# Kernel tuning notes

Measured on AMD Instinct MI355X. Metric: run time of the kernel, lower is better.

The kernel has to match this reference:

```python
import jax, jax.numpy as jnp
import numpy as np

N_NODES = 100000
N_EDGES = 1600000
NFEAT = 128
NHID = 128


def setup_inputs() -> dict:
    key = jax.random.key(0)
    k1, k2, k3, k4 = jax.random.split(key, 4)
    x = jax.random.normal(k1, (N_NODES, NFEAT), dtype=jnp.float32)
    edge_index = jax.random.randint(k2, (2, N_EDGES), 0, N_NODES, dtype=jnp.int64)
    # GCNConv params (glorot-style scale)
    W1 = jax.random.normal(k3, (NFEAT, NHID), dtype=jnp.float32) * (1.0 / np.sqrt(NFEAT))
    b1 = jnp.zeros((NHID,), dtype=jnp.float32)
    return {"x": x, "edge_index": edge_index, "W1": W1, "b1": b1}


def gcn_conv(x, edge_index, W, b):
    # PyG GCNConv: out = D^{-1/2} (A + I) D^{-1/2} (x W) + b
    n = x.shape[0]
    loop = jnp.arange(n, dtype=edge_index.dtype)
    src = jnp.concatenate([edge_index[0], loop])  # message sources
    dst = jnp.concatenate([edge_index[1], loop])  # aggregation targets
    deg = jax.ops.segment_sum(jnp.ones_like(dst, dtype=x.dtype), dst, num_segments=n)
    dinv = jnp.where(deg > 0, jax.lax.rsqrt(deg), 0.0)
    norm = dinv[src] * dinv[dst]  # [E+N]
    h = x @ W  # [N, nhid]
    msg = h[src] * norm[:, None]  # gather + scale, [E+N, nhid]
    out = jax.ops.segment_sum(msg, dst, num_segments=n) + b
    return out


def reference(x, edge_index, W1, b1):
    # forward = gc1(x, edge_index) followed by dropout (identity in eval mode)
    return gcn_conv(x, edge_index, W1, b1)
```

## Files before the change

### kernel.cpp

```cpp
#include <hip/hip_runtime.h>
#include <math.h>


#define N_NODES 100000
#define N_EDGES 1600000
#define NF 128

#define BSHIFT 7
#define BNODES 128
#define NBUCK 782
#define ECAP 2432
#define CHUNK 4096
#define NCHUNK 391
#define GEMM_BLOCKS 1563

typedef short bf16x8 __attribute__((ext_vector_type(8)));
typedef float f32x4  __attribute__((ext_vector_type(4)));
typedef unsigned short u16;

__device__ inline u16 f2bf(float f) {
    unsigned int u = __float_as_uint(f);
    return (u16)((u + 0x7fffu + ((u >> 16) & 1u)) >> 16);
}

__device__ inline f32x4 unpk4u(unsigned int u) {
    f32x4 r;
    r[0] = (float)(u & 0xffu);
    r[1] = (float)((u >> 8) & 0xffu);
    r[2] = (float)((u >> 16) & 0xffu);
    r[3] = (float)((u >> 24) & 0xffu);
    return r;
}

__global__ __launch_bounds__(256) void prep_kernel(const float* __restrict__ W,
                                                   u16* __restrict__ Wimg,
                                                   int* __restrict__ bcur) {
    const int t = threadIdx.x;
    if (blockIdx.x == 0)
        for (int b = t; b < NBUCK; b += 256) bcur[b] = 0;
    for (int idx = blockIdx.x * 256 + t; idx < NF * NF; idx += 16 * 256) {
        int n = idx >> 7, k = idx & 127;
        Wimg[idx] = f2bf(W[k * NF + n]);
    }
}

__global__ __launch_bounds__(256, 4) void fused1_kernel(const float* __restrict__ x,
                                                        const u16* __restrict__ Wimg,
                                                        signed char* __restrict__ h8,
                                                        float* __restrict__ rscale,
                                                        const int* __restrict__ ei,
                                                        int* __restrict__ bcur,
                                                        unsigned int* __restrict__ ebuf) {
    __shared__ __align__(16) char smem[22656];
    const int t = threadIdx.x;

    if (blockIdx.x >= GEMM_BLOCKS) {
        unsigned int* ed = (unsigned int*)smem;
        int* cnt = (int*)(smem + 16384);
        int* cur = (int*)(smem + 16384 + 3136);
        const int c = blockIdx.x - GEMM_BLOCKS;
        for (int b = t; b < NBUCK; b += 256) cnt[b] = 0;
        const int e0 = c * CHUNK;
        #pragma unroll 4
        for (int it = 0; it < CHUNK / 256; ++it) {
            int k = it * 256 + t, e = e0 + k;
            ed[k] = (e < N_EDGES) ? (unsigned int)ei[N_EDGES + e] : 0xFFFFFFFFu;
        }
        __syncthreads();
        #pragma unroll 4
        for (int it = 0; it < CHUNK / 256; ++it) {
            unsigned int d = ed[it * 256 + t];
            if (d != 0xFFFFFFFFu) atomicAdd(&cnt[d >> BSHIFT], 1);
        }
        __syncthreads();
        for (int b = t; b < NBUCK; b += 256) {
            int v = cnt[b];
            cur[b] = b * ECAP + (v ? atomicAdd(&bcur[b], v) : 0);
        }
        __syncthreads();
        #pragma unroll 4
        for (int it = 0; it < CHUNK / 256; ++it) {
            int k = it * 256 + t;
            unsigned int d = ed[k];
            if (d != 0xFFFFFFFFu) {
                int pos = atomicAdd(&cur[d >> BSHIFT], 1);
                ebuf[pos] = ((d & (BNODES - 1u)) << 17) | (unsigned int)ei[e0 + k];
            }
        }
        return;
    }

    const int lane = t & 63;
    const int w = t >> 6;
    const int quad = lane >> 4;
    const int m = lane & 15;
    const int rowbase = blockIdx.x * 64;
    const int r0 = w * 16;
    const int arow = rowbase + r0 + m;
    const bool rv = arow < N_NODES;
    const float4* x4 = (const float4*)x;

    f32x4 acc[8];
    #pragma unroll
    for (int nt = 0; nt < 8; ++nt) acc[nt] = (f32x4){0.f, 0.f, 0.f, 0.f};

    #pragma unroll
    for (int kt = 0; kt < 4; ++kt) {
        float4 xa = make_float4(0.f, 0.f, 0.f, 0.f), xb = xa;
        if (rv) {
            xa = x4[arow * 32 + kt * 8 + quad * 2];
            xb = x4[arow * 32 + kt * 8 + quad * 2 + 1];
        }
        bf16x8 a;
        a[0] = (short)f2bf(xa.x); a[1] = (short)f2bf(xa.y);
        a[2] = (short)f2bf(xa.z); a[3] = (short)f2bf(xa.w);
        a[4] = (short)f2bf(xb.x); a[5] = (short)f2bf(xb.y);
        a[6] = (short)f2bf(xb.z); a[7] = (short)f2bf(xb.w);
        #pragma unroll
        for (int nt = 0; nt < 8; ++nt) {
            bf16x8 bb = *(const bf16x8*)&Wimg[(nt * 16 + m) * NF + kt * 32 + quad * 8];
            acc[nt] = __builtin_amdgcn_mfma_f32_16x16x32_bf16(a, bb, acc[nt], 0, 0, 0);
        }
    }

    float rmax[4];
    #pragma unroll
    for (int r = 0; r < 4; ++r) {
        float mx = 0.f;
        #pragma unroll
        for (int nt = 0; nt < 8; ++nt) mx = fmaxf(mx, fabsf(acc[nt][r]));
        #pragma unroll
        for (int off = 1; off < 16; off <<= 1) mx = fmaxf(mx, __shfl_xor(mx, off));
        rmax[r] = fmaxf(mx, 1e-20f);
    }

    char* xs8 = smem;
    #pragma unroll
    for (int r = 0; r < 4; ++r) {
        const float inv = 127.f / rmax[r];
        const int row = r0 + quad * 4 + r;
        #pragma unroll
        for (int nt = 0; nt < 8; ++nt) {
            int q = __float2int_rn(acc[nt][r] * inv) + 128;
            xs8[row * 144 + nt * 16 + m] = (char)q;
        }
        if (m == 0) {
            int grow = rowbase + row;
            if (grow < N_NODES) rscale[grow] = rmax[r] * (1.f / 127.f);
        }
    }
    __syncthreads();

    for (int it = 0; it < 2; ++it) {
        int linear = it * 256 + t;
        int row = linear >> 3, seg = linear & 7;
        int grow = rowbase + row;
        if (grow < N_NODES) {
            uint4 v = *(const uint4*)&xs8[row * 144 + seg * 16];
            ((uint4*)h8)[grow * 8 + seg] = v;
        }
    }
}

__global__ __launch_bounds__(256) void fill3_kernel(unsigned int* __restrict__ ebuf,
                                                    const int* __restrict__ bcur,
                                                    const float* __restrict__ rscale,
                                                    float* __restrict__ combo,
                                                    int4* __restrict__ nodetab) {
    __shared__ unsigned int lde[ECAP];
    __shared__ int lcnt[BNODES];
    __shared__ int lsc[BNODES];
    __shared__ int lcur[BNODES];
    const int t = threadIdx.x, bkt = blockIdx.x;
    const int cnt = min(bcur[bkt], ECAP);
    const int gbase = bkt * ECAP;
    if (t < BNODES) lcnt[t] = 0;
    __syncthreads();
    for (int e = t; e < cnt; e += 256) {
        unsigned int p = ebuf[gbase + e];
        lde[e] = p;
        atomicAdd(&lcnt[p >> 17], 1);
    }
    __syncthreads();
    if (t < BNODES) lsc[t] = lcnt[t];
    __syncthreads();
    #pragma unroll
    for (int off = 1; off < BNODES; off <<= 1) {
        int v = (t < BNODES) ? lsc[t] : 0;
        int add = (t >= off && t < BNODES) ? lsc[t - off] : 0;
        __syncthreads();
        if (t < BNODES) lsc[t] = v + add;
        __syncthreads();
    }
    if (t < BNODES) {
        int c = lcnt[t];
        int startp = gbase + lsc[t] - c;
        lcur[t] = startp;
        int n = (bkt << BSHIFT) + t;
        if (n < N_NODES) {
            float dv = rsqrtf((float)c + 1.0f);
            float cb = dv * rscale[n];
            combo[n] = cb;
            nodetab[n] = make_int4(startp, c, __float_as_int(dv), __float_as_int(cb));
        }
    }
    __syncthreads();
    for (int e = t; e < cnt; e += 256) {
        unsigned int p = lde[e];
        int pos = atomicAdd(&lcur[p >> 17], 1);
        ebuf[pos] = p & 0x1ffffu;
    }
}

__global__ __launch_bounds__(256) void agg_kernel(const signed char* __restrict__ h8,
                                                  const float* __restrict__ combo,
                                                  const int4* __restrict__ nodetab,
                                                  const unsigned int* __restrict__ slot,
                                                  const float* __restrict__ b,
                                                  float* __restrict__ out) {
    const int wave = threadIdx.x >> 6;
    const int lane = threadIdx.x & 63;
    const int i = blockIdx.x * 4 + wave;
    if (i >= N_NODES) return;

    const int4 ni = nodetab[i];
    const int start = ni.x;
    const int m = ni.y;
    const float di = __int_as_float(ni.z);
    const float ci = __int_as_float(ni.w);
    const int half = lane >> 5;
    const int col = lane & 31;

    const unsigned int* h4 = (const unsigned int*)h8;
    f32x4 acc0 = {0.f, 0.f, 0.f, 0.f};
    f32x4 acc1 = {0.f, 0.f, 0.f, 0.f};
    float ws = 0.f;

    for (int base = 0; base < m; base += 64) {
        const int mm = min(m - base, 64);
        int   s_l  = (lane < mm) ? (int)slot[start + base + lane] : 0;
        float cw_l = (lane < mm) ? combo[s_l] : 0.0f;
        const int mu = (mm + 7) & ~7;
        for (int j = 0; j < mu; j += 8) {
            #pragma unroll
            for (int q = 0; q < 8; q += 2) {
                int   sj = __shfl(s_l,  j + q + half);
                float wj = __shfl(cw_l, j + q + half);
                unsigned int u = h4[sj * 32 + col];
                ws += wj;
                f32x4 hv = unpk4u(u);
                if (q & 2) acc1 += hv * wj;
                else       acc0 += hv * wj;
            }
        }
    }

    f32x4 acc = acc0 + acc1;
    #pragma unroll
    for (int c = 0; c < 4; ++c) acc[c] += __shfl_xor(acc[c], 32);
    ws += __shfl_xor(ws, 32);

    if (lane < 32) {
        unsigned int uv = h4[i * 32 + col];
        f32x4 hv = unpk4u(uv);
        float4 bb = ((const float4*)b)[col];
        const float corr = 128.f * (ws + ci);
        float4 o;
        o.x = bb.x + di * (acc[0] + ci * hv[0] - corr);
        o.y = bb.y + di * (acc[1] + ci * hv[1] - corr);
        o.z = bb.z + di * (acc[2] + ci * hv[2] - corr);
        o.w = bb.w + di * (acc[3] + ci * hv[3] - corr);
        ((float4*)out)[i * 32 + col] = o;
    }
}

extern "C" void kernel_launch(void* const* d_in, const int* in_sizes, int n_in,
                              void* d_out, int out_size, void* d_ws, size_t ws_size,
                              hipStream_t stream) {
    const float* x  = (const float*)d_in[0];
    const int*   ei = (const int*)d_in[1];
    const float* W  = (const float*)d_in[2];
    const float* b  = (const float*)d_in[3];
    float* out = (float*)d_out;

    signed char* h8 = (signed char*)d_ws;
    float* rscale = (float*)d_ws + 3300000;
    float* combo  = (float*)d_ws + 3500000;
    int4*  nodetab = (int4*)((int*)d_ws + 3700000);
    int*   bcur   = (int*)d_ws + 4150000;
    u16*   Wimg   = (u16*)((int*)d_ws + 4200000);
    unsigned int* ebuf = (unsigned int*)d_ws + 4300000;

    prep_kernel<<<16, 256, 0, stream>>>(W, Wimg, bcur);
    fused1_kernel<<<GEMM_BLOCKS + NCHUNK, 256, 0, stream>>>(x, Wimg, h8, rscale,
                                                            ei, bcur, ebuf);
    fill3_kernel<<<NBUCK, 256, 0, stream>>>(ebuf, bcur, rscale, combo, nodetab);
    agg_kernel<<<(N_NODES + 3) / 4, 256, 0, stream>>>(h8, combo, nodetab, ebuf, b, out);
}
```

Measured before the change: 219.6 us.

## Stage padded W in LDS, prefetch x rows, reorder edge-bucketing blocks first

The bf16 weight image is now stored with a padded row stride, and each GEMM block copies it into shared memory instead of reading B fragments from global memory. All x loads are issued up front before the MFMA loop. Edge-bucketing blocks now come first in the grid so they start early, and they stage source indices in LDS with coalesced loads. The aggregation inner loop is manually unrolled so the four gathers issue together. Shared memory grows to about 39 KB, which may lower occupancy of the fused kernel, and an extra barrier is added.

```diff
diff --git a/kernel.cpp b/kernel.cpp
--- a/kernel.cpp
+++ b/kernel.cpp
@@ -5,6 +5,7 @@
 #define N_NODES 100000
 #define N_EDGES 1600000
 #define NF 128
+#define LDW 136
 
 #define BSHIFT 7
 #define BNODES 128
@@ -28,7 +29,7 @@
     r[0] = (float)(u & 0xffu);
     r[1] = (float)((u >> 8) & 0xffu);
     r[2] = (float)((u >> 16) & 0xffu);
-    r[3] = (float)((u >> 24) & 0xffu);
+    r[3] = (float)(u >> 24);
     return r;
 }
 
@@ -40,7 +41,7 @@
         for (int b = t; b < NBUCK; b += 256) bcur[b] = 0;
     for (int idx = blockIdx.x * 256 + t; idx < NF * NF; idx += 16 * 256) {
         int n = idx >> 7, k = idx & 127;
-        Wimg[idx] = f2bf(W[k * NF + n]);
+        Wimg[n * LDW + k] = f2bf(W[k * NF + n]);
     }
 }
 
@@ -51,20 +52,24 @@
                                                         const int* __restrict__ ei,
                                                         int* __restrict__ bcur,
                                                         unsigned int* __restrict__ ebuf) {
-    __shared__ __align__(16) char smem[22656];
+    __shared__ __align__(16) char smem[39040];
     const int t = threadIdx.x;
 
-    if (blockIdx.x >= GEMM_BLOCKS) {
+    if (blockIdx.x < NCHUNK) {
         unsigned int* ed = (unsigned int*)smem;
-        int* cnt = (int*)(smem + 16384);
-        int* cur = (int*)(smem + 16384 + 3136);
-        const int c = blockIdx.x - GEMM_BLOCKS;
+        unsigned int* es = (unsigned int*)(smem + 16384);
+        int* cnt = (int*)(smem + 32768);
+        int* cur = (int*)(smem + 32768 + 3136);
+        const int c = blockIdx.x;
         for (int b = t; b < NBUCK; b += 256) cnt[b] = 0;
         const int e0 = c * CHUNK;
         #pragma unroll 4
         for (int it = 0; it < CHUNK / 256; ++it) {
             int k = it * 256 + t, e = e0 + k;
-            ed[k] = (e < N_EDGES) ? (unsigned int)ei[N_EDGES + e] : 0xFFFFFFFFu;
+            if (e < N_EDGES) {
+                ed[k] = (unsigned int)ei[N_EDGES + e];
+                es[k] = (unsigned int)ei[e];
+            } else ed[k] = 0xFFFFFFFFu;
         }
         __syncthreads();
         #pragma unroll 4
@@ -84,41 +89,54 @@
             unsigned int d = ed[k];
             if (d != 0xFFFFFFFFu) {
                 int pos = atomicAdd(&cur[d >> BSHIFT], 1);
-                ebuf[pos] = ((d & (BNODES - 1u)) << 17) | (unsigned int)ei[e0 + k];
+                ebuf[pos] = ((d & (BNODES - 1u)) << 17) | es[k];
             }
         }
         return;
     }
 
+    const int gb = blockIdx.x - NCHUNK;
     const int lane = t & 63;
     const int w = t >> 6;
     const int quad = lane >> 4;
     const int m = lane & 15;
-    const int rowbase = blockIdx.x * 64;
+    const int rowbase = gb * 64;
     const int r0 = w * 16;
     const int arow = rowbase + r0 + m;
     const bool rv = arow < N_NODES;
     const float4* x4 = (const float4*)x;
 
+    u16* Wt = (u16*)smem;
+    for (int idx = t; idx < (NF * LDW * 2) / 16; idx += 256)
+        ((uint4*)Wt)[idx] = ((const uint4*)Wimg)[idx];
+
+    float4 xr[8];
+    #pragma unroll
+    for (int kt = 0; kt < 4; ++kt) {
+        if (rv) {
+            xr[2 * kt]     = x4[arow * 32 + kt * 8 + quad * 2];
+            xr[2 * kt + 1] = x4[arow * 32 + kt * 8 + quad * 2 + 1];
+        } else {
+            xr[2 * kt] = make_float4(0.f, 0.f, 0.f, 0.f);
+            xr[2 * kt + 1] = make_float4(0.f, 0.f, 0.f, 0.f);
+        }
+    }
+    __syncthreads();
+
     f32x4 acc[8];
     #pragma unroll
     for (int nt = 0; nt < 8; ++nt) acc[nt] = (f32x4){0.f, 0.f, 0.f, 0.f};
 
     #pragma unroll
     for (int kt = 0; kt < 4; ++kt) {
-        float4 xa = make_float4(0.f, 0.f, 0.f, 0.f), xb = xa;
-        if (rv) {
-            xa = x4[arow * 32 + kt * 8 + quad * 2];
-            xb = x4[arow * 32 + kt * 8 + quad * 2 + 1];
-        }
         bf16x8 a;
-        a[0] = (short)f2bf(xa.x); a[1] = (short)f2bf(xa.y);
-        a[2] = (short)f2bf(xa.z); a[3] = (short)f2bf(xa.w);
-        a[4] = (short)f2bf(xb.x); a[5] = (short)f2bf(xb.y);
-        a[6] = (short)f2bf(xb.z); a[7] = (short)f2bf(xb.w);
+        a[0] = (short)f2bf(xr[2 * kt].x);     a[1] = (short)f2bf(xr[2 * kt].y);
+        a[2] = (short)f2bf(xr[2 * kt].z);     a[3] = (short)f2bf(xr[2 * kt].w);
+        a[4] = (short)f2bf(xr[2 * kt + 1].x); a[5] = (short)f2bf(xr[2 * kt + 1].y);
+        a[6] = (short)f2bf(xr[2 * kt + 1].z); a[7] = (short)f2bf(xr[2 * kt + 1].w);
         #pragma unroll
         for (int nt = 0; nt < 8; ++nt) {
-            bf16x8 bb = *(const bf16x8*)&Wimg[(nt * 16 + m) * NF + kt * 32 + quad * 8];
+            bf16x8 bb = *(const bf16x8*)&Wt[(nt * 16 + m) * LDW + kt * 32 + quad * 8];
             acc[nt] = __builtin_amdgcn_mfma_f32_16x16x32_bf16(a, bb, acc[nt], 0, 0, 0);
         }
     }
@@ -134,6 +152,7 @@
         rmax[r] = fmaxf(mx, 1e-20f);
     }
 
+    __syncthreads();
     char* xs8 = smem;
     #pragma unroll
     for (int r = 0; r < 4; ++r) {
@@ -242,16 +261,23 @@
         float cw_l = (lane < mm) ? combo[s_l] : 0.0f;
         const int mu = (mm + 7) & ~7;
         for (int j = 0; j < mu; j += 8) {
-            #pragma unroll
-            for (int q = 0; q < 8; q += 2) {
-                int   sj = __shfl(s_l,  j + q + half);
-                float wj = __shfl(cw_l, j + q + half);
-                unsigned int u = h4[sj * 32 + col];
-                ws += wj;
-                f32x4 hv = unpk4u(u);
-                if (q & 2) acc1 += hv * wj;
-                else       acc0 += hv * wj;
-            }
+            int sj0 = __shfl(s_l, j + 0 + half);
+            int sj1 = __shfl(s_l, j + 2 + half);
+            int sj2 = __shfl(s_l, j + 4 + half);
+            int sj3 = __shfl(s_l, j + 6 + half);
+            float wj0 = __shfl(cw_l, j + 0 + half);
+            float wj1 = __shfl(cw_l, j + 2 + half);
+            float wj2 = __shfl(cw_l, j + 4 + half);
+            float wj3 = __shfl(cw_l, j + 6 + half);
+            unsigned int u0 = h4[sj0 * 32 + col];
+            unsigned int u1 = h4[sj1 * 32 + col];
+            unsigned int u2 = h4[sj2 * 32 + col];
+            unsigned int u3 = h4[sj3 * 32 + col];
+            ws += wj0 + wj1 + wj2 + wj3;
+            acc0 += unpk4u(u0) * wj0;
+            acc1 += unpk4u(u1) * wj1;
+            acc0 += unpk4u(u2) * wj2;
+            acc1 += unpk4u(u3) * wj3;
         }
     }
 
@@ -292,7 +318,7 @@
     unsigned int* ebuf = (unsigned int*)d_ws + 4300000;
 
     prep_kernel<<<16, 256, 0, stream>>>(W, Wimg, bcur);
-    fused1_kernel<<<GEMM_BLOCKS + NCHUNK, 256, 0, stream>>>(x, Wimg, h8, rscale,
+    fused1_kernel<<<NCHUNK + GEMM_BLOCKS, 256, 0, stream>>>(x, Wimg, h8, rscale,
                                                             ei, bcur, ebuf);
     fill3_kernel<<<NBUCK, 256, 0, stream>>>(ebuf, bcur, rscale, combo, nodetab);
     agg_kernel<<<(N_NODES + 3) / 4, 256, 0, stream>>>(h8, combo, nodetab, ebuf, b, out);
```

Result: faster. 191.9 us (-12.6%).
